# Kernel tuning notes

Measured on AMD Instinct MI355X. Metric: run time of the kernel, lower is better.

## Reference

```python
import jax, jax.numpy as jnp
import numpy as np

N_EMBD = 1024
N_HEAD = 16
SEQ = 2048
BATCH = 2
NEG = -1000000000.0


def setup_inputs() -> dict:
    key = jax.random.key(0)
    k0, k1, k2 = jax.random.split(key, 3)
    return {
        "hidden_states": jax.random.normal(k0, (BATCH, SEQ, N_EMBD), dtype=jnp.float32),
        "w_attn": jax.random.normal(k1, (3 * N_EMBD, N_EMBD), dtype=jnp.float32) * 0.02,
        "b_attn": jnp.zeros((3 * N_EMBD,), dtype=jnp.float32),
        "w_proj": jax.random.normal(k2, (N_EMBD, N_EMBD), dtype=jnp.float32) * 0.02,
        "b_proj": jnp.zeros((N_EMBD,), dtype=jnp.float32),
    }


def reference(hidden_states, w_attn, b_attn, w_proj, b_proj):
    B, S, E = hidden_states.shape
    H = N_HEAD
    D = E // H
    # fused qkv projection (Conv1D: x @ kernel.T + bias)
    qkv = hidden_states @ w_attn.T + b_attn  # [B, S, 3E]
    q, k, v = jnp.split(qkv, 3, axis=-1)
    # split heads: [B, S, (H D)] -> [B, H, S, D]
    split = lambda t: t.reshape(B, S, H, D).transpose(0, 2, 1, 3)
    q, k, v = split(q), split(k), split(v)
    # scores [B, H, S, S]
    w = jnp.einsum("bhnd,bhmd->bhnm", q, k) * jax.lax.rsqrt(float(D))
    mask = jnp.tril(jnp.ones((S, S), dtype=jnp.float32))
    w = jnp.where(mask > 0, w, NEG)
    w = jax.nn.softmax(w, axis=-1)
    attn = jnp.einsum("bhnm,bhmd->bhnd", w, v)
    # merge heads -> [B, S, E]
    attn = attn.transpose(0, 2, 1, 3).reshape(B, S, E)
    return attn @ w_proj.T + b_proj
```

## Files before the change

### kernel.cpp

```cpp
#include <hip/hip_runtime.h>
#include <stdint.h>

#define S_LEN  2048
#define EMBD   1024
#define NHEAD  16
#define HDIM   64
#define BATCHN 2
#define ROWS   (BATCHN * S_LEN)

using bf16x8 = __attribute__((ext_vector_type(8))) __bf16;
using f32x4  = __attribute__((ext_vector_type(4))) float;
using f32x16 = __attribute__((ext_vector_type(16))) float;
using u32x4  = __attribute__((ext_vector_type(4))) unsigned;

typedef const __attribute__((address_space(1))) void* gas_ptr;
typedef __attribute__((address_space(3)))       void* las_ptr;

__device__ __forceinline__ void load_lds16(const void* g, void* l) {
    __builtin_amdgcn_global_load_lds((gas_ptr)(uintptr_t)g, (las_ptr)(uintptr_t)l, 16, 0, 0);
}

__device__ __forceinline__ unsigned short f2bf(float f) {
    unsigned u = __builtin_bit_cast(unsigned, f);
    u += 0x7fffu + ((u >> 16) & 1u);
    return (unsigned short)(u >> 16);
}

__device__ __forceinline__ unsigned pkbf(float a, float b) {
    unsigned r;
    asm("v_cvt_pk_bf16_f32 %0, %1, %2" : "=v"(r) : "v"(a), "v"(b));
    return r;
}

__device__ __forceinline__ int swz(int row, int ebase) {
    int byte = (row << 7) + (ebase << 1);
    byte ^= (row & 7) << 4;
    return byte >> 1;
}

__device__ __forceinline__ int swzV(int row, int ebase) {
    int byte = (row << 8) + (ebase << 1);
    byte ^= (row & 15) << 4;
    return byte >> 1;
}

__global__ void cvt3_f32_bf16(const float* __restrict__ s0,
                              const float* __restrict__ s1,
                              const float* __restrict__ s2,
                              unsigned short* __restrict__ d,
                              int n0, int n01, int ntot) {
    int i = blockIdx.x * blockDim.x + threadIdx.x;
    int stride = gridDim.x * blockDim.x;
    for (int idx = i * 4; idx < ntot; idx += stride * 4) {
        const float* s; int off;
        if (idx < n0)       { s = s0; off = idx; }
        else if (idx < n01) { s = s1; off = idx - n0; }
        else                { s = s2; off = idx - n01; }
        float4 f = *(const float4*)(s + off);
        uint2 p;
        p.x = (unsigned)f2bf(f.x) | ((unsigned)f2bf(f.y) << 16);
        p.y = (unsigned)f2bf(f.z) | ((unsigned)f2bf(f.w) << 16);
        *(uint2*)(d + idx) = p;
    }
}

#define SCALE_Q 0.18033688011112042f

__global__ __launch_bounds__(512, 2) void gemm_qkv(
    const unsigned short* __restrict__ A, const unsigned short* __restrict__ B,
    const float* __restrict__ bias,
    unsigned short* __restrict__ qb, unsigned short* __restrict__ kb,
    unsigned short* __restrict__ vb)
{
    __shared__ __align__(16) unsigned short sA[2][256 * 64];
    __shared__ __align__(16) unsigned short sB[2][192 * 64];

    const int tid  = threadIdx.x;
    const int wid  = tid >> 6;
    const int lane = tid & 63;
    const int g    = lane >> 4;
    const int c    = lane & 15;
    const int bm   = blockIdx.x * 256;
    const int bn   = blockIdx.y * 192;
    const int wm2  = (wid >> 2) * 128;
    const int wn2  = (wid & 3) * 48;
    const int K    = EMBD;
    const int NKT  = K / 64;

    f32x4 acc[8][3] = {};

    auto stage_a = [&](int kt, int buf) {
        const int k0 = kt * 64;
#pragma unroll
        for (int i = 0; i < 4; ++i) {
            int cbase = i * 512 + wid * 64;
            int cidx  = cbase + lane;
            int row   = cidx >> 3;
            int col   = ((cidx & 7) ^ (row & 7)) << 3;
            load_lds16(A + (size_t)(bm + row) * K + k0 + col, &sA[buf][cbase * 8]);
        }
    };
    auto stage_b = [&](int kt, int buf) {
        const int k0 = kt * 64;
#pragma unroll
        for (int i = 0; i < 3; ++i) {
            int cbase = i * 512 + wid * 64;
            int cidx  = cbase + lane;
            int row   = cidx >> 3;
            int col   = ((cidx & 7) ^ (row & 7)) << 3;
            load_lds16(B + (size_t)(bn + row) * K + k0 + col, &sB[buf][cbase * 8]);
        }
    };

    stage_a(0, 0);
    stage_b(0, 0);

    for (int kt = 0; kt < NKT; ++kt) {
        const int buf = kt & 1;
        asm volatile("s_waitcnt vmcnt(0)" ::: "memory");
        __builtin_amdgcn_s_barrier();

        bf16x8 bfr[3][2];
#pragma unroll
        for (int q = 0; q < 4; ++q) {
            if (kt + 1 < NKT) {
                if (q == 0) stage_a(kt + 1, buf ^ 1);
                if (q == 1) stage_b(kt + 1, buf ^ 1);
            }
            if (q == 0) {
#pragma unroll
                for (int j = 0; j < 3; ++j)
#pragma unroll
                    for (int kk = 0; kk < 2; ++kk)
                        bfr[j][kk] = *(const bf16x8*)
                            &sB[buf][swz(wn2 + j * 16 + c, kk * 32 + g * 8)];
            }
            bf16x8 af[2][2];
#pragma unroll
            for (int ii = 0; ii < 2; ++ii)
#pragma unroll
                for (int kk = 0; kk < 2; ++kk)
                    af[ii][kk] = *(const bf16x8*)
                        &sA[buf][swz(wm2 + (q * 2 + ii) * 16 + c, kk * 32 + g * 8)];

            __builtin_amdgcn_s_barrier();
            __builtin_amdgcn_s_setprio(1);
#pragma unroll
            for (int ii = 0; ii < 2; ++ii)
#pragma unroll
                for (int j = 0; j < 3; ++j)
#pragma unroll
                    for (int kk = 0; kk < 2; ++kk)
                        acc[q * 2 + ii][j] = __builtin_amdgcn_mfma_f32_16x16x32_bf16(
                            af[ii][kk], bfr[j][kk], acc[q * 2 + ii][j], 0, 0, 0);
            __builtin_amdgcn_s_setprio(0);
            __builtin_amdgcn_s_barrier();
        }
    }

    asm volatile("s_waitcnt vmcnt(0)" ::: "memory");

#pragma unroll
    for (int i = 0; i < 8; ++i)
#pragma unroll
        for (int j = 0; j < 3; ++j) {
            int n = bn + wn2 + j * 16 + c;
            float bv = bias[n];
            int which = n >> 10, h = (n & 1023) >> 6, d = n & 63;
            if (which < 2) {
                unsigned short* dst = (which == 0) ? qb : kb;
                float sc = (which == 0) ? SCALE_Q : 1.0f;
#pragma unroll
                for (int r = 0; r < 4; ++r) {
                    int m = bm + wm2 + i * 16 + g * 4 + r;
                    int b = m >> 11, s = m & 2047;
                    dst[(((size_t)b * NHEAD + h) * S_LEN + s) * HDIM + d] =
                        f2bf((acc[i][j][r] + bv) * sc);
                }
            } else {
                int m0 = bm + wm2 + i * 16 + g * 4;
                int b = m0 >> 11, s0 = m0 & 2047;
                uint2 p;
                p.x = pkbf(acc[i][j][0] + bv, acc[i][j][1] + bv);
                p.y = pkbf(acc[i][j][2] + bv, acc[i][j][3] + bv);
                *(uint2*)&vb[(((size_t)b * NHEAD + h) * HDIM + d) * S_LEN + s0] = p;
            }
        }
}

__global__ __launch_bounds__(256) void gemm_proj(
    const unsigned short* __restrict__ A, const unsigned short* __restrict__ B,
    const float* __restrict__ bias, float* __restrict__ Cout, int M, int N, int K)
{
    __shared__ __align__(16) unsigned short sA[128 * 64];
    __shared__ __align__(16) unsigned short sB[128 * 64];

    const int tid  = threadIdx.x;
    const int wid  = tid >> 6;
    const int lane = tid & 63;
    const int g    = lane >> 4;
    const int c    = lane & 15;
    const int bm   = blockIdx.x * 128;
    const int bn   = blockIdx.y * 128;
    const int wm   = (wid >> 1) * 64;
    const int wn   = (wid & 1) * 64;

    f32x4 acc[4][4] = {};

    for (int k0 = 0; k0 < K; k0 += 64) {
#pragma unroll
        for (int i = 0; i < 4; ++i) {
            int cidx = i * 256 + tid;
            int row  = cidx >> 3;
            int col  = ((cidx & 7) ^ (row & 7)) << 3;
            load_lds16(A + (size_t)(bm + row) * K + k0 + col,
                       &sA[i * 2048 + wid * 512]);
            load_lds16(B + (size_t)(bn + row) * K + k0 + col,
                       &sB[i * 2048 + wid * 512]);
        }
        __syncthreads();
#pragma unroll
        for (int kk = 0; kk < 2; ++kk) {
            bf16x8 af[4], bfr[4];
#pragma unroll
            for (int i = 0; i < 4; ++i)
                af[i] = *(const bf16x8*)&sA[swz(wm + i * 16 + c, kk * 32 + g * 8)];
#pragma unroll
            for (int j = 0; j < 4; ++j)
                bfr[j] = *(const bf16x8*)&sB[swz(wn + j * 16 + c, kk * 32 + g * 8)];
#pragma unroll
            for (int i = 0; i < 4; ++i)
#pragma unroll
                for (int j = 0; j < 4; ++j)
                    acc[i][j] = __builtin_amdgcn_mfma_f32_16x16x32_bf16(
                        af[i], bfr[j], acc[i][j], 0, 0, 0);
        }
        __syncthreads();
    }

#pragma unroll
    for (int i = 0; i < 4; ++i)
#pragma unroll
        for (int j = 0; j < 4; ++j) {
            int n = bn + wn + j * 16 + c;
            float bv = bias[n];
#pragma unroll
            for (int r = 0; r < 4; ++r) {
                int m = bm + wm + i * 16 + g * 4 + r;
                Cout[(size_t)m * N + n] = acc[i][j][r] + bv;
            }
        }
}

__global__ __launch_bounds__(512) void attn_kernel(
    const unsigned short* __restrict__ qbuf, const unsigned short* __restrict__ kbuf,
    const unsigned short* __restrict__ vtbuf, unsigned short* __restrict__ obuf)
{
    __shared__ __align__(16) unsigned short sK[3][128 * 64];
    __shared__ __align__(16) unsigned short sV[3][64 * 128];

    const int tid  = threadIdx.x;
    const int wid  = tid >> 6;
    const int wg   = wid & 3;
    const int grp  = wid >> 2;
    const int lane = tid & 63;
    const int hi   = lane >> 5;
    const int q5   = lane & 31;

    const int x  = blockIdx.x;
    const int jj = x >> 5;
    const int bh = x & 31;
    const int b  = bh >> 4, h = bh & 15;

    const int sH   = 15 - jj;
    const int sOwn = grp ? jj : sH;
    const int TT   = 16 - jj;

    const unsigned short* Qh = qbuf  + (size_t)bh * S_LEN * HDIM;
    const unsigned short* Kh = kbuf  + (size_t)bh * S_LEN * HDIM;
    const unsigned short* Vt = vtbuf + (size_t)bh * HDIM * S_LEN;

    const int diagOwn = 2 * sOwn + (wg >> 1);
    const int diagA   = 2 * sH + (wg >> 1);
    const int csplit  = 16 + (wg >> 1);
    const int qgOwn   = 128 * sOwn + 32 * wg + q5;
    const int qgSt    = 128 * sH + 32 * wg + q5;

    auto stage = [&](int t, int buf) {
#pragma unroll
        for (int i = 0; i < 4; ++i) {
            int cbase = wg * 256 + i * 64;
            int cidx  = cbase + lane;
            if (grp == 0) {
                int row = cidx >> 3, col = ((cidx & 7) ^ (row & 7)) << 3;
                load_lds16(Kh + (size_t)(t * 128 + row) * HDIM + col,
                           &sK[buf][cbase * 8]);
            } else {
                int row = cidx >> 4, col = ((cidx & 15) ^ (row & 15)) << 3;
                load_lds16(Vt + (size_t)row * S_LEN + t * 128 + col,
                           &sV[buf][cbase * 8]);
            }
        }
    };

    bf16x8 aq[4], aqS[4];
#pragma unroll
    for (int ks = 0; ks < 4; ++ks)
        aq[ks] = *(const bf16x8*)&Qh[(size_t)qgOwn * HDIM + ks * 16 + hi * 8];
    if (grp == 1) {
#pragma unroll
        for (int ks = 0; ks < 4; ++ks)
            aqS[ks] = *(const bf16x8*)&Qh[(size_t)qgSt * HDIM + ks * 16 + hi * 8];
    }

    f32x16 o2[2] = {}, oS[2] = {};
    float m_i = -1e30f, l_i = 0.f;
    float mS  = -1e30f, lS  = 0.f;

    auto tile64 = [&](int t64, int buf, int half, const bf16x8* aqv, int qgv,
                      int diagv, float& m, float& l, f32x16& oA, f32x16& oB) {
        f32x16 acc[2] = {};
        __builtin_amdgcn_s_setprio(1);
#pragma unroll
        for (int ks = 0; ks < 4; ++ks) {
            bf16x8 k0 = *(const bf16x8*)&sK[buf][swz(half * 64 + q5,      ks * 16 + hi * 8)];
            bf16x8 k1 = *(const bf16x8*)&sK[buf][swz(half * 64 + q5 + 32, ks * 16 + hi * 8)];
            acc[0] = __builtin_amdgcn_mfma_f32_32x32x16_bf16(k0, aqv[ks], acc[0], 0, 0, 0);
            acc[1] = __builtin_amdgcn_mfma_f32_32x32x16_bf16(k1, aqv[ks], acc[1], 0, 0, 0);
        }
        __builtin_amdgcn_s_setprio(0);

        if (t64 == diagv) {
#pragma unroll
            for (int t2 = 0; t2 < 2; ++t2) {
                int base = t64 * 64 + t2 * 32 + 4 * hi;
#pragma unroll
                for (int r = 0; r < 16; ++r)
                    if (base + (r & 3) + 8 * (r >> 2) > qgv) acc[t2][r] = -1e30f;
            }
        }

        float mx[8];
#pragma unroll
        for (int i = 0; i < 8; ++i)
            mx[i] = fmaxf(fmaxf(acc[i >> 2][(i & 3) * 4 + 0], acc[i >> 2][(i & 3) * 4 + 1]),
                          fmaxf(acc[i >> 2][(i & 3) * 4 + 2], acc[i >> 2][(i & 3) * 4 + 3]));
        float pm = fmaxf(fmaxf(fmaxf(mx[0], mx[1]), fmaxf(mx[2], mx[3])),
                         fmaxf(fmaxf(mx[4], mx[5]), fmaxf(mx[6], mx[7])));

        if (__any(pm > m + 8.0f)) {
            float pmr   = fmaxf(pm, __shfl_xor(pm, 32, 64));
            float m_new = fmaxf(m, pmr);
            float fac, dm = m - m_new;
            asm("v_exp_f32 %0, %1" : "=v"(fac) : "v"(dm));
            l *= fac;
            m  = m_new;
#pragma unroll
            for (int r = 0; r < 16; ++r) { oA[r] *= fac; oB[r] *= fac; }
        }

        unsigned pd[2][8];
        float lsum = 0.f;
#pragma unroll
        for (int t2 = 0; t2 < 2; ++t2) {
            float ev[16];
#pragma unroll
            for (int r = 0; r < 16; ++r) {
                float a = acc[t2][r] - m;
                asm("v_exp_f32 %0, %1" : "=v"(ev[r]) : "v"(a));
            }
            float s4[4];
#pragma unroll
            for (int u = 0; u < 4; ++u) {
                s4[u] = (ev[4 * u] + ev[4 * u + 1]) + (ev[4 * u + 2] + ev[4 * u + 3]);
                pd[t2][2 * u]     = pkbf(ev[4 * u],     ev[4 * u + 1]);
                pd[t2][2 * u + 1] = pkbf(ev[4 * u + 2], ev[4 * u + 3]);
            }
            lsum += (s4[0] + s4[1]) + (s4[2] + s4[3]);
        }
        l += lsum;

        __builtin_amdgcn_s_setprio(1);
#pragma unroll
        for (int ks = 0; ks < 4; ++ks) {
            const int t2 = ks >> 1, k1 = ks & 1;
            unsigned p0 = pd[t2][4 * k1 + 0], p1 = pd[t2][4 * k1 + 1];
            unsigned p2 = pd[t2][4 * k1 + 2], p3 = pd[t2][4 * k1 + 3];
            asm("v_permlane32_swap_b32 %0, %1" : "+v"(p0), "+v"(p2));
            asm("v_permlane32_swap_b32 %0, %1" : "+v"(p1), "+v"(p3));
            u32x4 fw;
            fw[0] = p0; fw[1] = p1; fw[2] = p2; fw[3] = p3;
            bf16x8 pf = __builtin_bit_cast(bf16x8, fw);
            bf16x8 v0 = *(const bf16x8*)&sV[buf][swzV(q5,      half * 64 + ks * 16 + hi * 8)];
            bf16x8 v1 = *(const bf16x8*)&sV[buf][swzV(q5 + 32, half * 64 + ks * 16 + hi * 8)];
            oA = __builtin_amdgcn_mfma_f32_32x32x16_bf16(v0, pf, oA, 0, 0, 0);
            oB = __builtin_amdgcn_mfma_f32_32x32x16_bf16(v1, pf, oB, 0, 0, 0);
        }
        __builtin_amdgcn_s_setprio(0);
    };

    stage(0, 0);
    stage(1, 1);

    for (int tt = 0; tt < TT; ++tt) {
        const int buf = tt % 3;
        asm volatile("s_waitcnt vmcnt(4)" ::: "memory");
        __builtin_amdgcn_s_barrier();
        stage(tt + 2 < TT ? tt + 2 : TT - 1, (tt + 2) % 3);

#pragma unroll
        for (int half = 0; half < 2; ++half) {
            const int t64 = 2 * tt + half;
            if (grp == 0) {
                if (t64 < csplit)
                    tile64(t64, buf, half, aq, qgOwn, -1, m_i, l_i, o2[0], o2[1]);
            } else {
                if (t64 <= diagOwn)
                    tile64(t64, buf, half, aq, qgOwn, diagOwn, m_i, l_i, o2[0], o2[1]);
                else if (t64 >= csplit && t64 <= diagA)
                    tile64(t64, buf, half, aqS, qgSt, diagA, mS, lS, oS[0], oS[1]);
            }
        }
    }

    asm volatile("s_waitcnt vmcnt(0)" ::: "memory");
    __builtin_amdgcn_s_barrier();

    float* mrg = (float*)&sK[0][0];
    if (grp == 1) {
        int base = (wg * 64 + lane) * 34;
#pragma unroll
        for (int t2 = 0; t2 < 2; ++t2)
#pragma unroll
            for (int r = 0; r < 16; ++r) mrg[base + t2 * 16 + r] = oS[t2][r];
        mrg[base + 32] = mS;
        mrg[base + 33] = lS;
    }
    __builtin_amdgcn_s_barrier();

    if (grp == 0) {
        int base = (wg * 64 + lane) * 34;
        float mB = mrg[base + 32], lB = mrg[base + 33];
        float mN = fmaxf(m_i, mB);
        float fA, fB, dA = m_i - mN, dB = mB - mN;
        asm("v_exp_f32 %0, %1" : "=v"(fA) : "v"(dA));
        asm("v_exp_f32 %0, %1" : "=v"(fB) : "v"(dB));
        l_i = l_i * fA + lB * fB;
#pragma unroll
        for (int t2 = 0; t2 < 2; ++t2)
#pragma unroll
            for (int r = 0; r < 16; ++r)
                o2[t2][r] = o2[t2][r] * fA + mrg[base + t2 * 16 + r] * fB;
    }

    float l_full = l_i + __shfl_xor(l_i, 32, 64);
    float rl = 1.0f / l_full;
    unsigned short* orow = &obuf[((size_t)(b * S_LEN + qgOwn)) * EMBD + h * HDIM];
#pragma unroll
    for (int t2 = 0; t2 < 2; ++t2)
#pragma unroll
        for (int u = 0; u < 4; ++u) {
            uint2 pw;
            pw.x = pkbf(o2[t2][4 * u] * rl,     o2[t2][4 * u + 1] * rl);
            pw.y = pkbf(o2[t2][4 * u + 2] * rl, o2[t2][4 * u + 3] * rl);
            *(uint2*)&orow[t2 * 32 + 4 * hi + 8 * u] = pw;
        }
}

extern "C" void kernel_launch(void* const* d_in, const int* in_sizes, int n_in,
                              void* d_out, int out_size, void* d_ws, size_t ws_size,
                              hipStream_t stream) {
    const float* hidden = (const float*)d_in[0];
    const float* w_attn = (const float*)d_in[1];
    const float* b_attn = (const float*)d_in[2];
    const float* w_proj = (const float*)d_in[3];
    const float* b_proj = (const float*)d_in[4];
    float* out = (float*)d_out;

    unsigned short* Xbf  = (unsigned short*)d_ws;
    unsigned short* Wabf = Xbf  + (size_t)ROWS * EMBD;
    unsigned short* Wpbf = Wabf + (size_t)3 * EMBD * EMBD;
    unsigned short* qb   = Wpbf + (size_t)EMBD * EMBD;
    unsigned short* kb   = qb + (size_t)BATCHN * NHEAD * S_LEN * HDIM;
    unsigned short* vtb  = kb + (size_t)BATCHN * NHEAD * S_LEN * HDIM;
    unsigned short* ob   = vtb + (size_t)BATCHN * NHEAD * S_LEN * HDIM;

    const int n0   = ROWS * EMBD;
    const int n01  = n0 + 3 * EMBD * EMBD;
    const int ntot = n01 + EMBD * EMBD;
    cvt3_f32_bf16<<<2048, 256, 0, stream>>>(hidden, w_attn, w_proj, Xbf,
                                            n0, n01, ntot);

    gemm_qkv<<<dim3(ROWS / 256, 3 * EMBD / 192), 512, 0, stream>>>(
        Xbf, Wabf, b_attn, qb, kb, vtb);

    attn_kernel<<<dim3(256), 512, 0, stream>>>(qb, kb, vtb, ob);

    gemm_proj<<<dim3(ROWS / 128, EMBD / 128), 256, 0, stream>>>(
        ob, Wpbf, b_proj, out, ROWS, EMBD, EMBD);
}
```

Before: 108.7 us.

## Interleave KV tiles between wave groups for both causal query blocks

Each attention workgroup handles a high and a low query block. Previously one wave group took the early KV tiles of the high block and the other took the low block plus the rest of the high block. Now both groups keep state for both blocks, and KV tiles alternate between groups by tile parity. Both partial results are merged through LDS at the end. The aim is a more even causal workload between the two groups, at the cost of more registers for a second Q fragment and accumulator set per wave.

```diff
diff --git a/kernel.cpp b/kernel.cpp
--- a/kernel.cpp
+++ b/kernel.cpp
@@ -272,19 +272,18 @@
     const int bh = x & 31;
     const int b  = bh >> 4, h = bh & 15;
 
-    const int sH   = 15 - jj;
-    const int sOwn = grp ? jj : sH;
-    const int TT   = 16 - jj;
+    const int sH = 15 - jj;
+    const int sL = jj;
+    const int TT = 16 - jj;
 
     const unsigned short* Qh = qbuf  + (size_t)bh * S_LEN * HDIM;
     const unsigned short* Kh = kbuf  + (size_t)bh * S_LEN * HDIM;
     const unsigned short* Vt = vtbuf + (size_t)bh * HDIM * S_LEN;
 
-    const int diagOwn = 2 * sOwn + (wg >> 1);
-    const int diagA   = 2 * sH + (wg >> 1);
-    const int csplit  = 16 + (wg >> 1);
-    const int qgOwn   = 128 * sOwn + 32 * wg + q5;
-    const int qgSt    = 128 * sH + 32 * wg + q5;
+    const int diagH = 2 * sH + (wg >> 1);
+    const int diagL = 2 * sL + (wg >> 1);
+    const int qgH   = 128 * sH + 32 * wg + q5;
+    const int qgL   = 128 * sL + 32 * wg + q5;
 
     auto stage = [&](int t, int buf) {
 #pragma unroll
@@ -303,19 +302,16 @@
         }
     };
 
-    bf16x8 aq[4], aqS[4];
-#pragma unroll
-    for (int ks = 0; ks < 4; ++ks)
-        aq[ks] = *(const bf16x8*)&Qh[(size_t)qgOwn * HDIM + ks * 16 + hi * 8];
-    if (grp == 1) {
-#pragma unroll
-        for (int ks = 0; ks < 4; ++ks)
-            aqS[ks] = *(const bf16x8*)&Qh[(size_t)qgSt * HDIM + ks * 16 + hi * 8];
-    }
-
-    f32x16 o2[2] = {}, oS[2] = {};
-    float m_i = -1e30f, l_i = 0.f;
-    float mS  = -1e30f, lS  = 0.f;
+    bf16x8 aqH[4], aqL[4];
+#pragma unroll
+    for (int ks = 0; ks < 4; ++ks) {
+        aqH[ks] = *(const bf16x8*)&Qh[(size_t)qgH * HDIM + ks * 16 + hi * 8];
+        aqL[ks] = *(const bf16x8*)&Qh[(size_t)qgL * HDIM + ks * 16 + hi * 8];
+    }
+
+    f32x16 oH[2] = {}, oL[2] = {};
+    float mH = -1e30f, lH = 0.f;
+    float mL = -1e30f, lL = 0.f;
 
     auto tile64 = [&](int t64, int buf, int half, const bf16x8* aqv, int qgv,
                       int diagv, float& m, float& l, f32x16& oA, f32x16& oB) {
@@ -411,14 +407,12 @@
 #pragma unroll
         for (int half = 0; half < 2; ++half) {
             const int t64 = 2 * tt + half;
-            if (grp == 0) {
-                if (t64 < csplit)
-                    tile64(t64, buf, half, aq, qgOwn, -1, m_i, l_i, o2[0], o2[1]);
+            if ((t64 & 1) == grp) {
+                if (t64 <= diagH)
+                    tile64(t64, buf, half, aqH, qgH, diagH, mH, lH, oH[0], oH[1]);
             } else {
-                if (t64 <= diagOwn)
-                    tile64(t64, buf, half, aq, qgOwn, diagOwn, m_i, l_i, o2[0], o2[1]);
-                else if (t64 >= csplit && t64 <= diagA)
-                    tile64(t64, buf, half, aqS, qgSt, diagA, mS, lS, oS[0], oS[1]);
+                if (t64 <= diagL)
+                    tile64(t64, buf, half, aqL, qgL, diagL, mL, lL, oL[0], oL[1]);
             }
         }
     }
@@ -426,43 +420,55 @@
     asm volatile("s_waitcnt vmcnt(0)" ::: "memory");
     __builtin_amdgcn_s_barrier();
 
-    float* mrg = (float*)&sK[0][0];
+    float* mrgH = (float*)&sK[0][0];
+    float* mrgL = (float*)&sV[0][0];
+    const int mbase = (wg * 64 + lane) * 34;
     if (grp == 1) {
-        int base = (wg * 64 + lane) * 34;
 #pragma unroll
         for (int t2 = 0; t2 < 2; ++t2)
 #pragma unroll
-            for (int r = 0; r < 16; ++r) mrg[base + t2 * 16 + r] = oS[t2][r];
-        mrg[base + 32] = mS;
-        mrg[base + 33] = lS;
+            for (int r = 0; r < 16; ++r) mrgH[mbase + t2 * 16 + r] = oH[t2][r];
+        mrgH[mbase + 32] = mH;
+        mrgH[mbase + 33] = lH;
+    } else {
+#pragma unroll
+        for (int t2 = 0; t2 < 2; ++t2)
+#pragma unroll
+            for (int r = 0; r < 16; ++r) mrgL[mbase + t2 * 16 + r] = oL[t2][r];
+        mrgL[mbase + 32] = mL;
+        mrgL[mbase + 33] = lL;
     }
     __builtin_amdgcn_s_barrier();
 
-    if (grp == 0) {
-        int base = (wg * 64 + lane) * 34;
-        float mB = mrg[base + 32], lB = mrg[base + 33];
-        float mN = fmaxf(m_i, mB);
-        float fA, fB, dA = m_i - mN, dB = mB - mN;
+    float* mrg = (grp == 0) ? mrgH : mrgL;
+    f32x16* oo = (grp == 0) ? oH : oL;
+    float mOwn = (grp == 0) ? mH : mL;
+    float lOwn = (grp == 0) ? lH : lL;
+    {
+        float mB = mrg[mbase + 32], lB = mrg[mbase + 33];
+        float mN = fmaxf(mOwn, mB);
+        float fA, fB, dA = mOwn - mN, dB = mB - mN;
         asm("v_exp_f32 %0, %1" : "=v"(fA) : "v"(dA));
         asm("v_exp_f32 %0, %1" : "=v"(fB) : "v"(dB));
-        l_i = l_i * fA + lB * fB;
+        lOwn = lOwn * fA + lB * fB;
 #pragma unroll
         for (int t2 = 0; t2 < 2; ++t2)
 #pragma unroll
             for (int r = 0; r < 16; ++r)
-                o2[t2][r] = o2[t2][r] * fA + mrg[base + t2 * 16 + r] * fB;
-    }
-
-    float l_full = l_i + __shfl_xor(l_i, 32, 64);
+                oo[t2][r] = oo[t2][r] * fA + mrg[mbase + t2 * 16 + r] * fB;
+    }
+
+    float l_full = lOwn + __shfl_xor(lOwn, 32, 64);
     float rl = 1.0f / l_full;
-    unsigned short* orow = &obuf[((size_t)(b * S_LEN + qgOwn)) * EMBD + h * HDIM];
+    const int qgOut = (grp == 0) ? qgH : qgL;
+    unsigned short* orow = &obuf[((size_t)(b * S_LEN + qgOut)) * EMBD + h * HDIM];
 #pragma unroll
     for (int t2 = 0; t2 < 2; ++t2)
 #pragma unroll
         for (int u = 0; u < 4; ++u) {
             uint2 pw;
-            pw.x = pkbf(o2[t2][4 * u] * rl,     o2[t2][4 * u + 1] * rl);
-            pw.y = pkbf(o2[t2][4 * u + 2] * rl, o2[t2][4 * u + 3] * rl);
+            pw.x = pkbf(oo[t2][4 * u] * rl,     oo[t2][4 * u + 1] * rl);
+            pw.y = pkbf(oo[t2][4 * u + 2] * rl, oo[t2][4 * u + 3] * rl);
             *(uint2*)&orow[t2 * 32 + 4 * hi + 8 * u] = pw;
         }
 }
```

Result: slower. 175.8 us (+61.8%).
